# Kernel optimization log

Measured on AMD Instinct MI355X. Metric: run time of the kernel, lower is better.

## Reference

```python
import jax, jax.numpy as jnp
import numpy as np

N_NODES = 100000


def _graph_conv(h, src_sl, dst_sl, out_norm, in_norm, W, b):
    # norm='both': h <- D_out^{-1/2} . A . D_in^{-1/2} . h . W + b
    h = h * out_norm[:, None]
    # gather source features over edges, scatter-sum into destinations (SpMM)
    agg = jax.ops.segment_sum(h[src_sl], dst_sl, num_segments=N_NODES)
    agg = agg * in_norm[:, None]
    return agg @ W + b


def setup_inputs() -> dict:
    key = jax.random.key(0)
    ks = jax.random.split(key, 8)
    n_edges = 1600000
    in_feats, n_hidden = 128, 64
    h = jax.random.normal(ks[0], (N_NODES, in_feats), dtype=jnp.float32)
    src = jax.random.randint(ks[1], (n_edges,), 0, N_NODES)
    dst = jax.random.randint(ks[2], (n_edges,), 0, N_NODES)
    dst_node_ids = jax.random.randint(ks[3], (1024,), 0, N_NODES)
    s_in = 1.0 / np.sqrt(in_feats)
    s_h = 1.0 / np.sqrt(n_hidden)
    W0 = jax.random.normal(ks[4], (in_feats, n_hidden), dtype=jnp.float32) * s_in
    W1 = jax.random.normal(ks[5], (n_hidden, n_hidden), dtype=jnp.float32) * s_h
    W2 = jax.random.normal(ks[6], (n_hidden, n_hidden), dtype=jnp.float32) * s_h
    b0 = jnp.zeros((n_hidden,), jnp.float32)
    b1 = jnp.zeros((n_hidden,), jnp.float32)
    b2 = jnp.zeros((n_hidden,), jnp.float32)
    return {"h": h, "src": src, "dst": dst, "dst_node_ids": dst_node_ids,
            "W0": W0, "b0": b0, "W1": W1, "b1": b1, "W2": W2, "b2": b2}


def reference(h, src, dst, dst_node_ids, W0, b0, W1, b1, W2, b2):
    # add_self_loop: append N self edges
    loops = jnp.arange(N_NODES, dtype=src.dtype)
    src_sl = jnp.concatenate([src, loops])
    dst_sl = jnp.concatenate([dst, loops])
    ones = jnp.ones_like(src_sl, dtype=jnp.float32)
    out_deg = jax.ops.segment_sum(ones, src_sl, num_segments=N_NODES)
    in_deg = jax.ops.segment_sum(ones, dst_sl, num_segments=N_NODES)
    out_norm = jax.lax.rsqrt(jnp.maximum(out_deg, 1.0))
    in_norm = jax.lax.rsqrt(jnp.maximum(in_deg, 1.0))
    h = h.astype(jnp.float32)
    # dropout p=0 -> identity between layers
    h = _graph_conv(h, src_sl, dst_sl, out_norm, in_norm, W0, b0)
    h = _graph_conv(h, src_sl, dst_sl, out_norm, in_norm, W1, b1)
    h = _graph_conv(h, src_sl, dst_sl, out_norm, in_norm, W2, b2)
    return h, dst_node_ids
```

## Files before the change

kernel.cpp:

```cpp
#include <hip/hip_runtime.h>

#define N_NODES 100000
#define FOUT 64

#define PSHIFT 9
#define PSIZE  512
#define NPART  ((N_NODES + PSIZE - 1) / PSIZE)
#define TILE   8192
#define SRCBITS 17
#define SRCMASK 0x1FFFF

#define SCAN_BLOCK 256
#define SCAN_ITEMS 8
#define SCAN_ELEMS (SCAN_BLOCK * SCAN_ITEMS)

typedef __attribute__((ext_vector_type(8))) short bf16x8;
typedef __attribute__((ext_vector_type(4))) float f32x4;
typedef __attribute__((ext_vector_type(2))) float f32x2;


static __device__ __forceinline__ float bf2f(unsigned short u) {
    union { unsigned int i; float f; } v;
    v.i = (unsigned int)u << 16;
    return v.f;
}
static __device__ __forceinline__ unsigned short f2bf(float f) {
    union { float f; unsigned int i; } v;
    v.f = f;
    unsigned int r = (v.i + 0x7fffu + ((v.i >> 16) & 1u)) >> 16;
    return (unsigned short)r;
}
static __device__ __forceinline__ unsigned int pk2(float x, float y) {
    return (unsigned int)f2bf(x) | ((unsigned int)f2bf(y) << 16);
}
static __device__ __forceinline__ f32x2 up2v(unsigned int u) {
    union { unsigned int i; float f; } lo, hi;
    lo.i = u << 16;
    hi.i = u & 0xffff0000u;
    f32x2 r; r[0] = lo.f; r[1] = hi.f;
    return r;
}

template <typename T> static __device__ __forceinline__ void stf(T* p, float v);
template <> __device__ __forceinline__ void stf<float>(float* p, float v) { *p = v; }
template <> __device__ __forceinline__ void stf<unsigned short>(unsigned short* p, float v) { *p = f2bf(v); }

static __device__ __forceinline__ void st2(float* base, int idx, float2 v) {
    ((float2*)base)[idx] = v;
}
static __device__ __forceinline__ void st2(unsigned short* base, int idx, float2 v) {
    ((unsigned int*)base)[idx] = pk2(v.x, v.y);
}

static __device__ __forceinline__ void st8(float* base, int d, int c4,
                                           const float4& r0, const float4& r1) {
    ((float4*)base)[(size_t)d * 16 + 2 * c4]     = r0;
    ((float4*)base)[(size_t)d * 16 + 2 * c4 + 1] = r1;
}
static __device__ __forceinline__ void st8(unsigned short* base, int d, int c4,
                                           const float4& r0, const float4& r1) {
    uint4 u;
    u.x = pk2(r0.x, r0.y); u.y = pk2(r0.z, r0.w);
    u.z = pk2(r1.x, r1.y); u.w = pk2(r1.z, r1.w);
    ((uint4*)base)[(size_t)d * 8 + c4] = u;
}

template <typename TIN> static __device__ __forceinline__ bf16x8 ldA(const TIN* p);
template <> __device__ __forceinline__ bf16x8 ldA<unsigned short>(const unsigned short* p) {
    return *(const bf16x8*)p;
}
template <> __device__ __forceinline__ bf16x8 ldA<float>(const float* p) {
    const f32x4* q = (const f32x4*)p;
    f32x4 lo = q[0], hi = q[1];
    bf16x8 a;
    a[0] = (short)f2bf(lo[0]); a[1] = (short)f2bf(lo[1]);
    a[2] = (short)f2bf(lo[2]); a[3] = (short)f2bf(lo[3]);
    a[4] = (short)f2bf(hi[0]); a[5] = (short)f2bf(hi[1]);
    a[6] = (short)f2bf(hi[2]); a[7] = (short)f2bf(hi[3]);
    return a;
}


__global__ void k_setup(const float* __restrict__ W0, const float* __restrict__ W1,
                        const float* __restrict__ W2,
                        unsigned short* __restrict__ Wt0, unsigned short* __restrict__ Wt1,
                        unsigned short* __restrict__ Wt2, unsigned int* __restrict__ tzero,
                        int* __restrict__ dstCur, int* __restrict__ srcCur, int capP,
                        const int* __restrict__ ids, float* __restrict__ outid, int nid) {
    int i = blockIdx.x * blockDim.x + threadIdx.x;
    if (i < 128 * 64) {
        int k = i >> 6, n = i & 63;
        Wt0[n * 128 + k] = f2bf(W0[i]);
    }
    if (i < 64 * 64) {
        int k = i >> 6, n = i & 63;
        Wt1[n * 64 + k] = f2bf(W1[i]);
        Wt2[n * 64 + k] = f2bf(W2[i]);
    }
    if (i < 32) tzero[i] = 0u;
    if (i < NPART) { dstCur[i] = i * capP; srcCur[i] = i * capP; }
    if (i < nid) outid[i] = (float)ids[i];
}


__global__ void __launch_bounds__(1024) k_binscatter(
        const int* __restrict__ src, const int* __restrict__ dst,
        int* __restrict__ dstCur, int* __restrict__ srcCur,
        unsigned int* __restrict__ dstStream,
        unsigned short* __restrict__ srcStream, int E) {
    __shared__ unsigned int   stageD[TILE];
    __shared__ unsigned short stageS[TILE];
    __shared__ int dh[NPART], sh2[NPART];
    __shared__ int dLoc[NPART], sLoc[NPART];
    __shared__ int dBase[NPART], sBase[NPART];
    __shared__ int dcur[NPART], scur[NPART];
    __shared__ int sbuf[256];

    const int tid = threadIdx.x;
    const int base = blockIdx.x * TILE;
    const int end = min(base + TILE, E);

    if (tid < NPART) { dh[tid] = 0; sh2[tid] = 0; }
    __syncthreads();

    for (int j = base + tid; j < end; j += 1024) {
        atomicAdd(&dh[dst[j] >> PSHIFT], 1);
        atomicAdd(&sh2[src[j] >> PSHIFT], 1);
    }
    __syncthreads();

    {
        int v = 0;
        if (tid < 256) { v = (tid < NPART) ? dh[tid] : 0; sbuf[tid] = v; }
        __syncthreads();
        for (int off = 1; off < 256; off <<= 1) {
            int x = 0;
            if (tid < 256 && tid >= off) x = sbuf[tid - off];
            __syncthreads();
            if (tid < 256) sbuf[tid] += x;
            __syncthreads();
        }
        if (tid < NPART) {
            int inc = sbuf[tid];
            dLoc[tid] = inc - v;
            dcur[tid] = inc - v;
            dBase[tid] = v ? atomicAdd(&dstCur[tid], v) : 0;
        }
        __syncthreads();
    }
    {
        int v = 0;
        if (tid < 256) { v = (tid < NPART) ? sh2[tid] : 0; sbuf[tid] = v; }
        __syncthreads();
        for (int off = 1; off < 256; off <<= 1) {
            int x = 0;
            if (tid < 256 && tid >= off) x = sbuf[tid - off];
            __syncthreads();
            if (tid < 256) sbuf[tid] += x;
            __syncthreads();
        }
        if (tid < NPART) {
            int inc = sbuf[tid];
            sLoc[tid] = inc - v;
            scur[tid] = inc - v;
            sBase[tid] = v ? atomicAdd(&srcCur[tid], v) : 0;
        }
        __syncthreads();
    }

    for (int j = base + tid; j < end; j += 1024) {
        int s = src[j], d = dst[j];
        int pd = atomicAdd(&dcur[d >> PSHIFT], 1);
        stageD[pd] = ((unsigned int)(d & (PSIZE - 1)) << SRCBITS) | (unsigned int)s;
        int ps = atomicAdd(&scur[s >> PSHIFT], 1);
        stageS[ps] = (unsigned short)(s & (PSIZE - 1));
    }
    __syncthreads();

    const int wv = tid >> 6;
    const int lane = tid & 63;
    for (int b = wv; b < NPART; b += 16) {
        const int cnt  = dh[b];
        const int loc  = dLoc[b];
        unsigned int* gd = dstStream + dBase[b];
        for (int i = lane; i < cnt; i += 64) gd[i] = stageD[loc + i];
        const int cnt2 = sh2[b];
        const int loc2 = sLoc[b];
        unsigned short* gs = srcStream + sBase[b];
        for (int i = lane; i < cnt2; i += 64) gs[i] = stageS[loc2 + i];
    }
}

__global__ void k_csr_odeg(const unsigned int* __restrict__ dstStream,
                           const unsigned short* __restrict__ srcStream,
                           const int* __restrict__ dstCur, const int* __restrict__ srcCur,
                           int capP,
                           int2* __restrict__ rowdeg, int* __restrict__ csr_src,
                           int* __restrict__ out_deg) {
    __shared__ int hist[PSIZE];
    __shared__ int part[PSIZE];
    const int tid = threadIdx.x;

    if (blockIdx.x < NPART) {
        const int p = blockIdx.x;
        const int nodeBase = p << PSHIFT;
        const int nN = min(PSIZE, N_NODES - nodeBase);
        const int e0 = p * capP;
        const int e1 = dstCur[p];

        for (int i = tid; i < PSIZE; i += 512) hist[i] = 0;
        __syncthreads();
        for (int e = e0 + tid; e < e1; e += 512)
            atomicAdd(&hist[dstStream[e] >> SRCBITS], 1);
        __syncthreads();

        int c = hist[tid];
        part[tid] = c;
        __syncthreads();
        for (int off = 1; off < PSIZE; off <<= 1) {
            int v = (tid >= off) ? part[tid - off] : 0;
            __syncthreads();
            part[tid] += v;
            __syncthreads();
        }
        int run = part[tid] - c;
        hist[tid] = run;
        if (tid < nN) rowdeg[nodeBase + tid] = make_int2(e0 + run, c);
        __syncthreads();

        for (int e = e0 + tid; e < e1; e += 512) {
            unsigned int rec = dstStream[e];
            int d = rec >> SRCBITS;
            int sv = rec & SRCMASK;
            int pos = atomicAdd(&hist[d], 1);
            csr_src[e0 + pos] = sv;
        }
    } else {
        const int p = blockIdx.x - NPART;
        const int nodeBase = p << PSHIFT;
        const int nN = min(PSIZE, N_NODES - nodeBase);
        const int e0 = p * capP;
        const int e1 = srcCur[p];

        for (int i = tid; i < PSIZE; i += 512) hist[i] = 0;
        __syncthreads();
        for (int e = e0 + tid; e < e1; e += 512)
            atomicAdd(&hist[srcStream[e]], 1);
        __syncthreads();
        if (tid < nN) out_deg[nodeBase + tid] = hist[tid];
    }
}

template <int FIN, typename TIN, typename TOUT>
__global__ void k_gemm_reg(const TIN* __restrict__ h, const int* __restrict__ out_deg,
                           const unsigned short* __restrict__ Wt, TOUT* __restrict__ t) {
    constexpr int NKC = FIN / 32;
    const int lane = threadIdx.x & 63;
    const int m = lane & 15;
    const int q = lane >> 4;
    const int wid = blockIdx.x * (blockDim.x >> 6) + (threadIdx.x >> 6);
    const int nw = (gridDim.x * blockDim.x) >> 6;
    const int nTiles = N_NODES / 16;

    bf16x8 bfrag[NKC][4];
#pragma unroll
    for (int kc = 0; kc < NKC; kc++)
#pragma unroll
        for (int nt = 0; nt < 4; nt++)
            bfrag[kc][nt] = *(const bf16x8*)&Wt[(nt * 16 + m) * FIN + kc * 32 + q * 8];

    for (int tile = wid; tile < nTiles; tile += nw) {
        const TIN* hrow = h + (size_t)(tile * 16 + m) * FIN + q * 8;
        f32x4 acc[4];
#pragma unroll
        for (int nt = 0; nt < 4; nt++) acc[nt] = (f32x4){0.f, 0.f, 0.f, 0.f};
#pragma unroll
        for (int kc = 0; kc < NKC; kc++) {
            bf16x8 a = ldA(hrow + kc * 32);
#pragma unroll
            for (int nt = 0; nt < 4; nt++)
                acc[nt] = __builtin_amdgcn_mfma_f32_16x16x32_bf16(a, bfrag[kc][nt], acc[nt], 0, 0, 0);
        }
        const int r0 = tile * 16 + q * 4;
        int4 dg = *(const int4*)&out_deg[r0];
        float s0 = rsqrtf((float)(dg.x + 1));
        float s1 = rsqrtf((float)(dg.y + 1));
        float s2 = rsqrtf((float)(dg.z + 1));
        float s3 = rsqrtf((float)(dg.w + 1));
#pragma unroll
        for (int nt = 0; nt < 4; nt++) {
            TOUT* tp = t + (size_t)r0 * FOUT + nt * 16 + m;
            stf(tp + 0 * FOUT, acc[nt][0] * s0);
            stf(tp + 1 * FOUT, acc[nt][1] * s1);
            stf(tp + 2 * FOUT, acc[nt][2] * s2);
            stf(tp + 3 * FOUT, acc[nt][3] * s3);
        }
    }
}


static __device__ __forceinline__ void accum8(f32x2* a, uint4 v) {
    a[0] += up2v(v.x);
    a[1] += up2v(v.y);
    a[2] += up2v(v.z);
    a[3] += up2v(v.w);
}

template <int G>
static __device__ __forceinline__ void chunk_full8(
        const uint4* __restrict__ t4, const int* __restrict__ bk,
        int base, int sub, int c4, f32x2* acc) {
    int s[G];
#pragma unroll
    for (int u = 0; u < G; u++) s[u] = bk[base + sub + 8 * u];
    uint4 v[G];
#pragma unroll
    for (int u = 0; u < G; u++) v[u] = t4[(size_t)s[u] * 8 + c4];
#pragma unroll
    for (int u = 0; u < G; u++) accum8(acc, v[u]);
}

template <int G>
static __device__ __forceinline__ void chunk_masked8(
        const uint4* __restrict__ t4, const int* __restrict__ bk,
        int base, int sub, int c4, int deg, int d, f32x2* acc) {
    int s[G];
#pragma unroll
    for (int u = 0; u < G; u++) {
        int i = base + sub + 8 * u;
        int sv = bk[i];
        s[u] = (i < deg) ? sv : ((i == deg) ? d : N_NODES);
    }
    uint4 v[G];
#pragma unroll
    for (int u = 0; u < G; u++) v[u] = t4[(size_t)s[u] * 8 + c4];
#pragma unroll
    for (int u = 0; u < G; u++) accum8(acc, v[u]);
}

template <typename TOUT>
__global__ void k_spmm_b(const uint4* __restrict__ t4,
                         const int2* __restrict__ rowdeg, const int* __restrict__ csr_src,
                         const float* __restrict__ bias, TOUT* __restrict__ out) {
    const int wave = blockIdx.x * (blockDim.x >> 6) + (threadIdx.x >> 6);
    const int lane = threadIdx.x & 63;
    const int sub = lane >> 3;
    const int c4 = lane & 7;
    const int d = wave;
    const int2 rd = rowdeg[d];
    const int e0 = rd.x;
    const int deg = rd.y;
    const float inorm = rsqrtf((float)(deg + 1));
    const int* bk = csr_src + e0;
    const int vdeg = deg + 1;

    f32x2 a[4];
#pragma unroll
    for (int j = 0; j < 4; j++) a[j] = (f32x2){0.f, 0.f};

    int base = 0;
    while (vdeg - base > 32) {
        chunk_full8<4>(t4, bk, base, sub, c4, a);
        base += 32;
    }
    if (vdeg - base > 16)
        chunk_masked8<4>(t4, bk, base, sub, c4, deg, d, a);
    else
        chunk_masked8<2>(t4, bk, base, sub, c4, deg, d, a);

#pragma unroll
    for (int off = 8; off < 64; off <<= 1) {
#pragma unroll
        for (int j = 0; j < 4; j++) {
            a[j][0] += __shfl_xor(a[j][0], off);
            a[j][1] += __shfl_xor(a[j][1], off);
        }
    }

    if (sub == 0) {
        const float4* b4 = (const float4*)bias;
        float4 bb0 = b4[2 * c4], bb1 = b4[2 * c4 + 1];
        float4 r0, r1;
        r0.x = inorm * a[0][0] + bb0.x;
        r0.y = inorm * a[0][1] + bb0.y;
        r0.z = inorm * a[1][0] + bb0.z;
        r0.w = inorm * a[1][1] + bb0.w;
        r1.x = inorm * a[2][0] + bb1.x;
        r1.y = inorm * a[2][1] + bb1.y;
        r1.z = inorm * a[3][0] + bb1.z;
        r1.w = inorm * a[3][1] + bb1.w;
        st8(out, d, c4, r0, r1);
    }
}


__global__ void k_init_fb(int* __restrict__ a, int* __restrict__ b,
                          const int* __restrict__ ids, float* __restrict__ outid,
                          int n, int nid) {
    int i = blockIdx.x * blockDim.x + threadIdx.x;
    if (i < n) { a[i] = 0; b[i] = 0; }
    if (i < nid) outid[i] = (float)ids[i];
}

__global__ void k_histo(const int* __restrict__ src, const int* __restrict__ dst,
                        int* __restrict__ out_deg, int* __restrict__ in_deg, int n) {
    int i = blockIdx.x * blockDim.x + threadIdx.x;
    if (i < n) {
        atomicAdd(&out_deg[src[i]], 1);
        atomicAdd(&in_deg[dst[i]], 1);
    }
}

__global__ void k_scan_partial(const int* __restrict__ deg, int* __restrict__ block_sums, int n) {
    __shared__ int red[SCAN_BLOCK];
    const int t = threadIdx.x;
    const int base = blockIdx.x * SCAN_ELEMS + t * SCAN_ITEMS;
    int s = 0;
#pragma unroll
    for (int k = 0; k < SCAN_ITEMS; k++) {
        int i = base + k;
        if (i < n) s += deg[i];
    }
    red[t] = s;
    __syncthreads();
    for (int off = SCAN_BLOCK / 2; off > 0; off >>= 1) {
        if (t < off) red[t] += red[t + off];
        __syncthreads();
    }
    if (t == 0) block_sums[blockIdx.x] = red[0];
}

__global__ void k_scan_blocks(int* __restrict__ block_sums, int nb) {
    __shared__ int sh[SCAN_BLOCK];
    const int t = threadIdx.x;
    sh[t] = (t < nb) ? block_sums[t] : 0;
    __syncthreads();
    for (int off = 1; off < SCAN_BLOCK; off <<= 1) {
        int v = (t >= off) ? sh[t - off] : 0;
        __syncthreads();
        sh[t] += v;
        __syncthreads();
    }
    if (t < nb) block_sums[t] = (t == 0) ? 0 : sh[t - 1];
}

__global__ void k_scan_write(const int* __restrict__ deg, const int* __restrict__ block_off,
                             int* __restrict__ row_off, int* __restrict__ cursor, int n) {
    __shared__ int sh[SCAN_BLOCK];
    const int t = threadIdx.x;
    const int base = blockIdx.x * SCAN_ELEMS + t * SCAN_ITEMS;
    int v[SCAN_ITEMS];
    int s = 0;
#pragma unroll
    for (int k = 0; k < SCAN_ITEMS; k++) {
        int i = base + k;
        v[k] = (i < n) ? deg[i] : 0;
        s += v[k];
    }
    sh[t] = s;
    __syncthreads();
    for (int off = 1; off < SCAN_BLOCK; off <<= 1) {
        int x = (t >= off) ? sh[t - off] : 0;
        __syncthreads();
        sh[t] += x;
        __syncthreads();
    }
    int run = block_off[blockIdx.x] + ((t == 0) ? 0 : sh[t - 1]);
#pragma unroll
    for (int k = 0; k < SCAN_ITEMS; k++) {
        int i = base + k;
        if (i < n) { row_off[i] = run; cursor[i] = run; run += v[k]; }
    }
    if (blockIdx.x == gridDim.x - 1 && t == SCAN_BLOCK - 1) {
        row_off[n] = block_off[blockIdx.x] + sh[SCAN_BLOCK - 1];
    }
}

__global__ void k_scatter(const int* __restrict__ src, const int* __restrict__ dst,
                          int* __restrict__ cursor, int* __restrict__ csr_src, int n) {
    int i = blockIdx.x * blockDim.x + threadIdx.x;
    if (i < n) {
        int d = dst[i];
        int pos = atomicAdd(&cursor[d], 1);
        csr_src[pos] = src[i];
    }
}

template <int FIN>
__global__ void k_gemm_fb(const float* __restrict__ h, const int* __restrict__ out_deg,
                          const float* __restrict__ W, float* __restrict__ t) {
    __shared__ float sh[32 * FIN];
    __shared__ float sno[32];
    const int tid = threadIdx.x;
    const int block0 = blockIdx.x * 32;

    if (tid < 32) sno[tid] = rsqrtf((float)(out_deg[block0 + tid] + 1));
    __syncthreads();

    for (int idx = tid; idx < 32 * FIN; idx += 256) {
        int r = idx / FIN;
        int c = idx % FIN;
        sh[idx] = h[(size_t)(block0 + r) * FIN + c] * sno[r];
    }
    __syncthreads();

    const int j2 = tid & 31;
    const int rg = tid >> 5;
    const float2* W2 = (const float2*)W;
    float2 a0 = {0.f, 0.f}, a1 = {0.f, 0.f}, a2 = {0.f, 0.f}, a3 = {0.f, 0.f};
#pragma unroll 4
    for (int k = 0; k < FIN; k++) {
        float2 w = W2[k * 32 + j2];
        float s0 = sh[(rg + 0)  * FIN + k];
        float s1 = sh[(rg + 8)  * FIN + k];
        float s2 = sh[(rg + 16) * FIN + k];
        float s3 = sh[(rg + 24) * FIN + k];
        a0.x += s0 * w.x; a0.y += s0 * w.y;
        a1.x += s1 * w.x; a1.y += s1 * w.y;
        a2.x += s2 * w.x; a2.y += s2 * w.y;
        a3.x += s3 * w.x; a3.y += s3 * w.y;
    }
    float* tp = t + (size_t)block0 * FOUT;
    st2(tp, (rg + 0)  * 32 + j2, a0);
    st2(tp, (rg + 8)  * 32 + j2, a1);
    st2(tp, (rg + 16) * 32 + j2, a2);
    st2(tp, (rg + 24) * 32 + j2, a3);
}

__global__ void k_spmm_c(const float* __restrict__ t, const int* __restrict__ row_off,
                         const int* __restrict__ csr_src, const float* __restrict__ bias,
                         float* __restrict__ out) {
    const int wave = blockIdx.x * (blockDim.x >> 6) + (threadIdx.x >> 6);
    const int lane = threadIdx.x & 63;
    const int d = wave;
    const int e0 = row_off[d];
    const int e1 = row_off[d + 1];
    const float inorm = rsqrtf((float)(e1 - e0 + 1));

    float a0 = t[(size_t)d * FOUT + lane];
    float a1 = 0.f, a2 = 0.f, a3 = 0.f, a4 = 0.f, a5 = 0.f, a6 = 0.f, a7 = 0.f;
    int e = e0;
    for (; e + 8 <= e1; e += 8) {
        int s0 = csr_src[e + 0], s1 = csr_src[e + 1], s2 = csr_src[e + 2], s3 = csr_src[e + 3];
        int s4 = csr_src[e + 4], s5 = csr_src[e + 5], s6 = csr_src[e + 6], s7 = csr_src[e + 7];
        a0 += t[(size_t)s0 * FOUT + lane];
        a1 += t[(size_t)s1 * FOUT + lane];
        a2 += t[(size_t)s2 * FOUT + lane];
        a3 += t[(size_t)s3 * FOUT + lane];
        a4 += t[(size_t)s4 * FOUT + lane];
        a5 += t[(size_t)s5 * FOUT + lane];
        a6 += t[(size_t)s6 * FOUT + lane];
        a7 += t[(size_t)s7 * FOUT + lane];
    }
    for (; e + 4 <= e1; e += 4) {
        int s0 = csr_src[e + 0], s1 = csr_src[e + 1], s2 = csr_src[e + 2], s3 = csr_src[e + 3];
        a0 += t[(size_t)s0 * FOUT + lane];
        a1 += t[(size_t)s1 * FOUT + lane];
        a2 += t[(size_t)s2 * FOUT + lane];
        a3 += t[(size_t)s3 * FOUT + lane];
    }
    for (; e < e1; e++) a0 += t[(size_t)csr_src[e] * FOUT + lane];

    float acc = ((a0 + a1) + (a2 + a3)) + ((a4 + a5) + (a6 + a7));
    out[(size_t)d * FOUT + lane] = inorm * acc + bias[lane];
}


extern "C" void kernel_launch(void* const* d_in, const int* in_sizes, int n_in,
                              void* d_out, int out_size, void* d_ws, size_t ws_size,
                              hipStream_t stream) {
    const float* h   = (const float*)d_in[0];
    const int*   src = (const int*)d_in[1];
    const int*   dst = (const int*)d_in[2];
    const int*   ids = (const int*)d_in[3];
    const float* W0  = (const float*)d_in[4];
    const float* b0  = (const float*)d_in[5];
    const float* W1  = (const float*)d_in[6];
    const float* b1  = (const float*)d_in[7];
    const float* W2  = (const float*)d_in[8];
    const float* b2  = (const float*)d_in[9];
    const int N = N_NODES;
    const int E = in_sizes[1];

    size_t o = 0;
    auto alloc = [&](size_t nbytes) -> void* {
        void* p = (char*)d_ws + o;
        o += (nbytes + 255) & ~(size_t)255;
        return p;
    };

    float* outp = (float*)d_out;
    const int B = 256;
    const int spmmGrid = N / 4;
    const int gemmGrid = (N / 16 + 3) / 4;

    const int capP = (((E / NPART) * 9) / 8 + 512 + 255) & ~255;
    const size_t streamEnt = (size_t)NPART * capP;

    const size_t needNew =
        ((streamEnt * 4 + 255) & ~(size_t)255) +
        ((streamEnt * 2 + 255) & ~(size_t)255) +
        ((streamEnt * 4 + 255) & ~(size_t)255) +
        (((size_t)N * 8 + 255) & ~(size_t)255) +
        (((size_t)N * 4 + 255) & ~(size_t)255) +
        2 * 1024 +
        2 * (((size_t)(N + 1) * FOUT * 2 + 255) & ~(size_t)255) +
        64 * 1024 + 4096;

    if (ws_size >= needNew) {
        unsigned int*   dstStream = (unsigned int*)alloc(streamEnt * 4);
        unsigned short* srcStream = (unsigned short*)alloc(streamEnt * 2);
        int*            csr_src   = (int*)alloc(streamEnt * 4);
        int2*           rowdeg    = (int2*)alloc((size_t)N * 8);
        int*            out_deg   = (int*)alloc((size_t)N * 4);
        int*            dstCur    = (int*)alloc(1024);
        int*            srcCur    = (int*)alloc(1024);
        unsigned short* t         = (unsigned short*)alloc((size_t)(N + 1) * FOUT * 2);
        unsigned short* hbuf      = (unsigned short*)alloc((size_t)N * FOUT * 2);
        unsigned short* Wt0       = (unsigned short*)alloc(128 * 64 * 2);
        unsigned short* Wt1       = (unsigned short*)alloc(64 * 64 * 2);
        unsigned short* Wt2       = (unsigned short*)alloc(64 * 64 * 2);

        const int nTiles = (E + TILE - 1) / TILE;

        k_setup<<<32, B, 0, stream>>>(W0, W1, W2, Wt0, Wt1, Wt2,
                                      (unsigned int*)(t + (size_t)N * FOUT),
                                      dstCur, srcCur, capP,
                                      ids, outp + (size_t)N * FOUT, 1024);
        k_binscatter<<<nTiles, 1024, 0, stream>>>(src, dst, dstCur, srcCur, dstStream, srcStream, E);
        k_csr_odeg<<<2 * NPART, 512, 0, stream>>>(dstStream, srcStream, dstCur, srcCur, capP,
                                                  rowdeg, csr_src, out_deg);

        k_gemm_reg<128, float, unsigned short><<<gemmGrid, B, 0, stream>>>(h, out_deg, Wt0, t);
        k_spmm_b<unsigned short><<<spmmGrid, B, 0, stream>>>((const uint4*)t, rowdeg, csr_src, b0, hbuf);
        k_gemm_reg<64, unsigned short, unsigned short><<<gemmGrid, B, 0, stream>>>(hbuf, out_deg, Wt1, t);
        k_spmm_b<unsigned short><<<spmmGrid, B, 0, stream>>>((const uint4*)t, rowdeg, csr_src, b1, hbuf);
        k_gemm_reg<64, unsigned short, unsigned short><<<gemmGrid, B, 0, stream>>>(hbuf, out_deg, Wt2, t);
        k_spmm_b<float><<<spmmGrid, B, 0, stream>>>((const uint4*)t, rowdeg, csr_src, b2, outp);
    } else {
        int*   in_deg  = (int*)alloc((size_t)N * 4);
        int*   out_deg = (int*)alloc((size_t)N * 4);
        int*   row_off = (int*)alloc((size_t)(N + 1) * 4);
        int*   cursor  = (int*)alloc((size_t)N * 4);
        int*   csr_src = (int*)alloc((size_t)E * 4);
        float* t       = (float*)alloc((size_t)N * FOUT * 4);
        float* hbuf    = (float*)alloc((size_t)N * FOUT * 4);
        int*   bsums   = (int*)alloc((size_t)SCAN_BLOCK * 4);

        const int gN = (N + B - 1) / B;
        const int gE = (E + B - 1) / B;
        const int nScanBlocks = (N + SCAN_ELEMS - 1) / SCAN_ELEMS;

        k_init_fb<<<gN, B, 0, stream>>>(in_deg, out_deg, ids, outp + (size_t)N * FOUT, N, 1024);
        k_histo<<<gE, B, 0, stream>>>(src, dst, out_deg, in_deg, E);
        k_scan_partial<<<nScanBlocks, SCAN_BLOCK, 0, stream>>>(in_deg, bsums, N);
        k_scan_blocks<<<1, SCAN_BLOCK, 0, stream>>>(bsums, nScanBlocks);
        k_scan_write<<<nScanBlocks, SCAN_BLOCK, 0, stream>>>(in_deg, bsums, row_off, cursor, N);
        k_scatter<<<gE, B, 0, stream>>>(src, dst, cursor, csr_src, E);

        k_gemm_fb<128><<<N / 32, 256, 0, stream>>>(h, out_deg, W0, t);
        k_spmm_c<<<spmmGrid, 256, 0, stream>>>(t, row_off, csr_src, b0, hbuf);
        k_gemm_fb<64><<<N / 32, 256, 0, stream>>>(hbuf, out_deg, W1, t);
        k_spmm_c<<<spmmGrid, 256, 0, stream>>>(t, row_off, csr_src, b1, hbuf);
        k_gemm_fb<64><<<N / 32, 256, 0, stream>>>(hbuf, out_deg, W2, t);
        k_spmm_c<<<spmmGrid, 256, 0, stream>>>(t, row_off, csr_src, b2, outp);
    }
}
```

Baseline: 305.6 us.

## Compute out-degree with global atomics instead of a partitioned src stream

Drops the source-side binning (the srcStream, its scan and scatter in k_binscatter, and the histogram half of k_csr_odeg) and replaces it with a separate k_odeg kernel that does vectorized global atomicAdd on out_deg, which is now zeroed in k_setup. The aim is to cut the shared-memory staging and stream writes and reads for the src side. The trade is about 1.6M global atomics spread over random addresses, plus one more kernel launch. The tail of the SpMM masked chunk is also split into finer sizes (1/2/3/4) so fewer idle lanes are processed.

```diff
diff --git a/kernel.cpp b/kernel.cpp
--- a/kernel.cpp
+++ b/kernel.cpp
@@ -85,7 +85,7 @@
                         const float* __restrict__ W2,
                         unsigned short* __restrict__ Wt0, unsigned short* __restrict__ Wt1,
                         unsigned short* __restrict__ Wt2, unsigned int* __restrict__ tzero,
-                        int* __restrict__ dstCur, int* __restrict__ srcCur, int capP,
+                        int* __restrict__ dstCur, int capP, int* __restrict__ out_deg,
                         const int* __restrict__ ids, float* __restrict__ outid, int nid) {
     int i = blockIdx.x * blockDim.x + threadIdx.x;
     if (i < 128 * 64) {
@@ -98,35 +98,46 @@
         Wt2[n * 64 + k] = f2bf(W2[i]);
     }
     if (i < 32) tzero[i] = 0u;
-    if (i < NPART) { dstCur[i] = i * capP; srcCur[i] = i * capP; }
+    if (i < NPART) dstCur[i] = i * capP;
+    if (i < N_NODES) out_deg[i] = 0;
     if (i < nid) outid[i] = (float)ids[i];
+}
+
+__global__ void k_odeg(const int* __restrict__ src, int* __restrict__ out_deg, int E) {
+    int i = blockIdx.x * blockDim.x + threadIdx.x;
+    int j = i * 4;
+    if (j + 4 <= E) {
+        int4 s = *(const int4*)&src[j];
+        atomicAdd(&out_deg[s.x], 1);
+        atomicAdd(&out_deg[s.y], 1);
+        atomicAdd(&out_deg[s.z], 1);
+        atomicAdd(&out_deg[s.w], 1);
+    } else {
+        for (; j < E; j++) atomicAdd(&out_deg[src[j]], 1);
+    }
 }
 
 
 __global__ void __launch_bounds__(1024) k_binscatter(
         const int* __restrict__ src, const int* __restrict__ dst,
-        int* __restrict__ dstCur, int* __restrict__ srcCur,
-        unsigned int* __restrict__ dstStream,
-        unsigned short* __restrict__ srcStream, int E) {
-    __shared__ unsigned int   stageD[TILE];
-    __shared__ unsigned short stageS[TILE];
-    __shared__ int dh[NPART], sh2[NPART];
-    __shared__ int dLoc[NPART], sLoc[NPART];
-    __shared__ int dBase[NPART], sBase[NPART];
-    __shared__ int dcur[NPART], scur[NPART];
+        int* __restrict__ dstCur,
+        unsigned int* __restrict__ dstStream, int E) {
+    __shared__ unsigned int stageD[TILE];
+    __shared__ int dh[NPART];
+    __shared__ int dLoc[NPART];
+    __shared__ int dBase[NPART];
+    __shared__ int dcur[NPART];
     __shared__ int sbuf[256];
 
     const int tid = threadIdx.x;
     const int base = blockIdx.x * TILE;
     const int end = min(base + TILE, E);
 
-    if (tid < NPART) { dh[tid] = 0; sh2[tid] = 0; }
-    __syncthreads();
-
-    for (int j = base + tid; j < end; j += 1024) {
+    if (tid < NPART) dh[tid] = 0;
+    __syncthreads();
+
+    for (int j = base + tid; j < end; j += 1024)
         atomicAdd(&dh[dst[j] >> PSHIFT], 1);
-        atomicAdd(&sh2[src[j] >> PSHIFT], 1);
-    }
     __syncthreads();
 
     {
@@ -148,106 +159,63 @@
         }
         __syncthreads();
     }
-    {
-        int v = 0;
-        if (tid < 256) { v = (tid < NPART) ? sh2[tid] : 0; sbuf[tid] = v; }
-        __syncthreads();
-        for (int off = 1; off < 256; off <<= 1) {
-            int x = 0;
-            if (tid < 256 && tid >= off) x = sbuf[tid - off];
-            __syncthreads();
-            if (tid < 256) sbuf[tid] += x;
-            __syncthreads();
-        }
-        if (tid < NPART) {
-            int inc = sbuf[tid];
-            sLoc[tid] = inc - v;
-            scur[tid] = inc - v;
-            sBase[tid] = v ? atomicAdd(&srcCur[tid], v) : 0;
-        }
-        __syncthreads();
-    }
 
     for (int j = base + tid; j < end; j += 1024) {
         int s = src[j], d = dst[j];
         int pd = atomicAdd(&dcur[d >> PSHIFT], 1);
         stageD[pd] = ((unsigned int)(d & (PSIZE - 1)) << SRCBITS) | (unsigned int)s;
-        int ps = atomicAdd(&scur[s >> PSHIFT], 1);
-        stageS[ps] = (unsigned short)(s & (PSIZE - 1));
     }
     __syncthreads();
 
     const int wv = tid >> 6;
     const int lane = tid & 63;
     for (int b = wv; b < NPART; b += 16) {
-        const int cnt  = dh[b];
-        const int loc  = dLoc[b];
+        const int cnt = dh[b];
+        const int loc = dLoc[b];
         unsigned int* gd = dstStream + dBase[b];
         for (int i = lane; i < cnt; i += 64) gd[i] = stageD[loc + i];
-        const int cnt2 = sh2[b];
-        const int loc2 = sLoc[b];
-        unsigned short* gs = srcStream + sBase[b];
-        for (int i = lane; i < cnt2; i += 64) gs[i] = stageS[loc2 + i];
-    }
-}
-
-__global__ void k_csr_odeg(const unsigned int* __restrict__ dstStream,
-                           const unsigned short* __restrict__ srcStream,
-                           const int* __restrict__ dstCur, const int* __restrict__ srcCur,
-                           int capP,
-                           int2* __restrict__ rowdeg, int* __restrict__ csr_src,
-                           int* __restrict__ out_deg) {
+    }
+}
+
+__global__ void k_csr(const unsigned int* __restrict__ dstStream,
+                      const int* __restrict__ dstCur, int capP,
+                      int2* __restrict__ rowdeg, int* __restrict__ csr_src) {
     __shared__ int hist[PSIZE];
     __shared__ int part[PSIZE];
     const int tid = threadIdx.x;
 
-    if (blockIdx.x < NPART) {
-        const int p = blockIdx.x;
-        const int nodeBase = p << PSHIFT;
-        const int nN = min(PSIZE, N_NODES - nodeBase);
-        const int e0 = p * capP;
-        const int e1 = dstCur[p];
-
-        for (int i = tid; i < PSIZE; i += 512) hist[i] = 0;
-        __syncthreads();
-        for (int e = e0 + tid; e < e1; e += 512)
-            atomicAdd(&hist[dstStream[e] >> SRCBITS], 1);
-        __syncthreads();
-
-        int c = hist[tid];
-        part[tid] = c;
-        __syncthreads();
-        for (int off = 1; off < PSIZE; off <<= 1) {
-            int v = (tid >= off) ? part[tid - off] : 0;
-            __syncthreads();
-            part[tid] += v;
-            __syncthreads();
-        }
-        int run = part[tid] - c;
-        hist[tid] = run;
-        if (tid < nN) rowdeg[nodeBase + tid] = make_int2(e0 + run, c);
-        __syncthreads();
-
-        for (int e = e0 + tid; e < e1; e += 512) {
-            unsigned int rec = dstStream[e];
-            int d = rec >> SRCBITS;
-            int sv = rec & SRCMASK;
-            int pos = atomicAdd(&hist[d], 1);
-            csr_src[e0 + pos] = sv;
-        }
-    } else {
-        const int p = blockIdx.x - NPART;
-        const int nodeBase = p << PSHIFT;
-        const int nN = min(PSIZE, N_NODES - nodeBase);
-        const int e0 = p * capP;
-        const int e1 = srcCur[p];
-
-        for (int i = tid; i < PSIZE; i += 512) hist[i] = 0;
-        __syncthreads();
-        for (int e = e0 + tid; e < e1; e += 512)
-            atomicAdd(&hist[srcStream[e]], 1);
-        __syncthreads();
-        if (tid < nN) out_deg[nodeBase + tid] = hist[tid];
+    const int p = blockIdx.x;
+    const int nodeBase = p << PSHIFT;
+    const int nN = min(PSIZE, N_NODES - nodeBase);
+    const int e0 = p * capP;
+    const int e1 = dstCur[p];
+
+    for (int i = tid; i < PSIZE; i += 512) hist[i] = 0;
+    __syncthreads();
+    for (int e = e0 + tid; e < e1; e += 512)
+        atomicAdd(&hist[dstStream[e] >> SRCBITS], 1);
+    __syncthreads();
+
+    int c = hist[tid];
+    part[tid] = c;
+    __syncthreads();
+    for (int off = 1; off < PSIZE; off <<= 1) {
+        int v = (tid >= off) ? part[tid - off] : 0;
+        __syncthreads();
+        part[tid] += v;
+        __syncthreads();
+    }
+    int run = part[tid] - c;
+    hist[tid] = run;
+    if (tid < nN) rowdeg[nodeBase + tid] = make_int2(e0 + run, c);
+    __syncthreads();
+
+    for (int e = e0 + tid; e < e1; e += 512) {
+        unsigned int rec = dstStream[e];
+        int d = rec >> SRCBITS;
+        int sv = rec & SRCMASK;
+        int pos = atomicAdd(&hist[d], 1);
+        csr_src[e0 + pos] = sv;
     }
 }
 
@@ -363,10 +331,13 @@
         chunk_full8<4>(t4, bk, base, sub, c4, a);
         base += 32;
     }
-    if (vdeg - base > 16)
-        chunk_masked8<4>(t4, bk, base, sub, c4, deg, d, a);
-    else
-        chunk_masked8<2>(t4, bk, base, sub, c4, deg, d, a);
+    {
+        const int rem = vdeg - base;
+        if (rem > 24)      chunk_masked8<4>(t4, bk, base, sub, c4, deg, d, a);
+        else if (rem > 16) chunk_masked8<3>(t4, bk, base, sub, c4, deg, d, a);
+        else if (rem > 8)  chunk_masked8<2>(t4, bk, base, sub, c4, deg, d, a);
+        else               chunk_masked8<1>(t4, bk, base, sub, c4, deg, d, a);
+    }
 
 #pragma unroll
     for (int off = 8; off < 64; off <<= 1) {
@@ -599,22 +570,19 @@
 
     const size_t needNew =
         ((streamEnt * 4 + 255) & ~(size_t)255) +
-        ((streamEnt * 2 + 255) & ~(size_t)255) +
         ((streamEnt * 4 + 255) & ~(size_t)255) +
         (((size_t)N * 8 + 255) & ~(size_t)255) +
         (((size_t)N * 4 + 255) & ~(size_t)255) +
-        2 * 1024 +
+        1024 +
         2 * (((size_t)(N + 1) * FOUT * 2 + 255) & ~(size_t)255) +
         64 * 1024 + 4096;
 
     if (ws_size >= needNew) {
         unsigned int*   dstStream = (unsigned int*)alloc(streamEnt * 4);
-        unsigned short* srcStream = (unsigned short*)alloc(streamEnt * 2);
         int*            csr_src   = (int*)alloc(streamEnt * 4);
         int2*           rowdeg    = (int2*)alloc((size_t)N * 8);
         int*            out_deg   = (int*)alloc((size_t)N * 4);
         int*            dstCur    = (int*)alloc(1024);
-        int*            srcCur    = (int*)alloc(1024);
         unsigned short* t         = (unsigned short*)alloc((size_t)(N + 1) * FOUT * 2);
         unsigned short* hbuf      = (unsigned short*)alloc((size_t)N * FOUT * 2);
         unsigned short* Wt0       = (unsigned short*)alloc(128 * 64 * 2);
@@ -623,13 +591,13 @@
 
         const int nTiles = (E + TILE - 1) / TILE;
 
-        k_setup<<<32, B, 0, stream>>>(W0, W1, W2, Wt0, Wt1, Wt2,
-                                      (unsigned int*)(t + (size_t)N * FOUT),
-                                      dstCur, srcCur, capP,
-                                      ids, outp + (size_t)N * FOUT, 1024);
-        k_binscatter<<<nTiles, 1024, 0, stream>>>(src, dst, dstCur, srcCur, dstStream, srcStream, E);
-        k_csr_odeg<<<2 * NPART, 512, 0, stream>>>(dstStream, srcStream, dstCur, srcCur, capP,
-                                                  rowdeg, csr_src, out_deg);
+        k_setup<<<(N + B - 1) / B, B, 0, stream>>>(W0, W1, W2, Wt0, Wt1, Wt2,
+                                                   (unsigned int*)(t + (size_t)N * FOUT),
+                                                   dstCur, capP, out_deg,
+                                                   ids, outp + (size_t)N * FOUT, 1024);
+        k_odeg<<<(E / 4 + B - 1) / B, B, 0, stream>>>(src, out_deg, E);
+        k_binscatter<<<nTiles, 1024, 0, stream>>>(src, dst, dstCur, dstStream, E);
+        k_csr<<<NPART, 512, 0, stream>>>(dstStream, dstCur, capP, rowdeg, csr_src);
 
         k_gemm_reg<128, float, unsigned short><<<gemmGrid, B, 0, stream>>>(h, out_deg, Wt0, t);
         k_spmm_b<unsigned short><<<spmmGrid, B, 0, stream>>>((const uint4*)t, rowdeg, csr_src, b0, hbuf);
```

Result: slower. 362.3 us (+18.6%).

## Use wave-shuffle scans and bake self-loops into CSR rows

Applied to the files above, without the earlier changes.

Replaces the shared-memory Hillis-Steele scans in the binning and CSR-build kernels with wave-level shuffle scans plus a small cross-wave fixup, which removes many block-wide barriers. The CSR build now writes each node's self-loop as an explicit entry, so the SpMM kernel drops its per-edge self-loop special case and uses finer-grained masked tail chunks (1-4 groups). Partition capacity is enlarged to make room for the extra self-loop entries. The setup kernels are small, so most of any effect depends on the SpMM tail handling.

```diff
diff --git a/kernel.cpp b/kernel.cpp
--- a/kernel.cpp
+++ b/kernel.cpp
@@ -78,6 +78,15 @@
     a[4] = (short)f2bf(hi[0]); a[5] = (short)f2bf(hi[1]);
     a[6] = (short)f2bf(hi[2]); a[7] = (short)f2bf(hi[3]);
     return a;
+}
+
+static __device__ __forceinline__ int wave_iscan(int x, int lane) {
+#pragma unroll
+    for (int off = 1; off < 64; off <<= 1) {
+        int y = __shfl_up(x, off);
+        if (lane >= off) x += y;
+    }
+    return x;
 }
 
 
@@ -114,9 +123,11 @@
     __shared__ int dLoc[NPART], sLoc[NPART];
     __shared__ int dBase[NPART], sBase[NPART];
     __shared__ int dcur[NPART], scur[NPART];
-    __shared__ int sbuf[256];
+    __shared__ int sbufD[4], sbufS[4];
 
     const int tid = threadIdx.x;
+    const int lane = tid & 63;
+    const int w = tid >> 6;
     const int base = blockIdx.x * TILE;
     const int end = min(base + TILE, E);
 
@@ -130,40 +141,23 @@
     __syncthreads();
 
     {
-        int v = 0;
-        if (tid < 256) { v = (tid < NPART) ? dh[tid] : 0; sbuf[tid] = v; }
-        __syncthreads();
-        for (int off = 1; off < 256; off <<= 1) {
-            int x = 0;
-            if (tid < 256 && tid >= off) x = sbuf[tid - off];
-            __syncthreads();
-            if (tid < 256) sbuf[tid] += x;
-            __syncthreads();
-        }
+        int vD = 0, vS = 0;
+        if (tid < NPART) { vD = dh[tid]; vS = sh2[tid]; }
+        int xD = wave_iscan(vD, lane);
+        int xS = wave_iscan(vS, lane);
+        if (tid < 256 && lane == 63) { sbufD[w] = xD; sbufS[w] = xS; }
+        __syncthreads();
         if (tid < NPART) {
-            int inc = sbuf[tid];
-            dLoc[tid] = inc - v;
-            dcur[tid] = inc - v;
-            dBase[tid] = v ? atomicAdd(&dstCur[tid], v) : 0;
-        }
-        __syncthreads();
-    }
-    {
-        int v = 0;
-        if (tid < 256) { v = (tid < NPART) ? sh2[tid] : 0; sbuf[tid] = v; }
-        __syncthreads();
-        for (int off = 1; off < 256; off <<= 1) {
-            int x = 0;
-            if (tid < 256 && tid >= off) x = sbuf[tid - off];
-            __syncthreads();
-            if (tid < 256) sbuf[tid] += x;
-            __syncthreads();
-        }
-        if (tid < NPART) {
-            int inc = sbuf[tid];
-            sLoc[tid] = inc - v;
-            scur[tid] = inc - v;
-            sBase[tid] = v ? atomicAdd(&srcCur[tid], v) : 0;
+            int addD = 0, addS = 0;
+            for (int j = 0; j < w; j++) { addD += sbufD[j]; addS += sbufS[j]; }
+            int incD = xD + addD;
+            int incS = xS + addS;
+            dLoc[tid] = incD - vD;
+            dcur[tid] = incD - vD;
+            dBase[tid] = vD ? atomicAdd(&dstCur[tid], vD) : 0;
+            sLoc[tid] = incS - vS;
+            scur[tid] = incS - vS;
+            sBase[tid] = vS ? atomicAdd(&srcCur[tid], vS) : 0;
         }
         __syncthreads();
     }
@@ -177,9 +171,7 @@
     }
     __syncthreads();
 
-    const int wv = tid >> 6;
-    const int lane = tid & 63;
-    for (int b = wv; b < NPART; b += 16) {
+    for (int b = w; b < NPART; b += 16) {
         const int cnt  = dh[b];
         const int loc  = dLoc[b];
         unsigned int* gd = dstStream + dBase[b];
@@ -198,7 +190,7 @@
                            int2* __restrict__ rowdeg, int* __restrict__ csr_src,
                            int* __restrict__ out_deg) {
     __shared__ int hist[PSIZE];
-    __shared__ int part[PSIZE];
+    __shared__ int sbuf8[8];
     const int tid = threadIdx.x;
 
     if (blockIdx.x < NPART) {
@@ -214,18 +206,21 @@
             atomicAdd(&hist[dstStream[e] >> SRCBITS], 1);
         __syncthreads();
 
+        const int lane = tid & 63;
+        const int w = tid >> 6;
         int c = hist[tid];
-        part[tid] = c;
-        __syncthreads();
-        for (int off = 1; off < PSIZE; off <<= 1) {
-            int v = (tid >= off) ? part[tid - off] : 0;
-            __syncthreads();
-            part[tid] += v;
-            __syncthreads();
+        int v = c + 1;
+        int x = wave_iscan(v, lane);
+        if (lane == 63) sbuf8[w] = x;
+        __syncthreads();
+        int add = 0;
+        for (int j = 0; j < w; j++) add += sbuf8[j];
+        int run = x + add - v;
+        hist[tid] = run + 1;
+        if (tid < nN) {
+            rowdeg[nodeBase + tid] = make_int2(e0 + run, v);
+            csr_src[e0 + run] = nodeBase + tid;
         }
-        int run = part[tid] - c;
-        hist[tid] = run;
-        if (tid < nN) rowdeg[nodeBase + tid] = make_int2(e0 + run, c);
         __syncthreads();
 
         for (int e = e0 + tid; e < e1; e += 512) {
@@ -323,13 +318,13 @@
 template <int G>
 static __device__ __forceinline__ void chunk_masked8(
         const uint4* __restrict__ t4, const int* __restrict__ bk,
-        int base, int sub, int c4, int deg, int d, f32x2* acc) {
+        int base, int sub, int c4, int vdeg, f32x2* acc) {
     int s[G];
 #pragma unroll
     for (int u = 0; u < G; u++) {
         int i = base + sub + 8 * u;
         int sv = bk[i];
-        s[u] = (i < deg) ? sv : ((i == deg) ? d : N_NODES);
+        s[u] = (i < vdeg) ? sv : N_NODES;
     }
     uint4 v[G];
 #pragma unroll
@@ -349,10 +344,9 @@
     const int d = wave;
     const int2 rd = rowdeg[d];
     const int e0 = rd.x;
-    const int deg = rd.y;
-    const float inorm = rsqrtf((float)(deg + 1));
+    const int vdeg = rd.y;
+    const float inorm = rsqrtf((float)vdeg);
     const int* bk = csr_src + e0;
-    const int vdeg = deg + 1;
 
     f32x2 a[4];
 #pragma unroll
@@ -363,10 +357,13 @@
         chunk_full8<4>(t4, bk, base, sub, c4, a);
         base += 32;
     }
-    if (vdeg - base > 16)
-        chunk_masked8<4>(t4, bk, base, sub, c4, deg, d, a);
-    else
-        chunk_masked8<2>(t4, bk, base, sub, c4, deg, d, a);
+    {
+        const int rem = vdeg - base;
+        if (rem > 24)      chunk_masked8<4>(t4, bk, base, sub, c4, vdeg, a);
+        else if (rem > 16) chunk_masked8<3>(t4, bk, base, sub, c4, vdeg, a);
+        else if (rem > 8)  chunk_masked8<2>(t4, bk, base, sub, c4, vdeg, a);
+        else               chunk_masked8<1>(t4, bk, base, sub, c4, vdeg, a);
+    }
 
 #pragma unroll
     for (int off = 8; off < 64; off <<= 1) {
@@ -594,7 +591,7 @@
     const int spmmGrid = N / 4;
     const int gemmGrid = (N / 16 + 3) / 4;
 
-    const int capP = (((E / NPART) * 9) / 8 + 512 + 255) & ~255;
+    const int capP = (((E / NPART) * 9) / 8 + 1024 + 255) & ~255;
     const size_t streamEnt = (size_t)NPART * capP;
 
     const size_t needNew =
```

Result: faster. 295.2 us (-3.4%).
